# Kernel tuning notes

Measured on AMD Instinct MI355X. Metric: run time of the kernel, lower is better.

Reference implementation:

```python
import jax, jax.numpy as jnp
import numpy as np

NUM_HEADS = 12
LN_EPS = 1e-5


def _layernorm(t, w, b):
    # LayerNorm over last dim (head_dim), biased variance as in torch
    mu = jnp.mean(t, axis=-1, keepdims=True)
    var = jnp.mean(jnp.square(t - mu), axis=-1, keepdims=True)
    return (t - mu) * jax.lax.rsqrt(var + LN_EPS) * w + b


def _apply_rope(t, cos, sin):
    # t: [B, H, S, D]; cos/sin: [S, D//2]; interleaved complex pairs (torch view_as_complex)
    tr = t[..., 0::2]
    ti = t[..., 1::2]
    c = cos[None, None, :, :]
    s = sin[None, None, :, :]
    out_r = tr * c - ti * s
    out_i = tr * s + ti * c
    return jnp.stack([out_r, out_i], axis=-1).reshape(t.shape)


def setup_inputs() -> dict:
    key = jax.random.key(0)
    ks = jax.random.split(key, 6)
    B, N, C = 16, 1024, 768
    H = NUM_HEADS
    D = C // H  # 64
    P, L = 1, 32
    rot_len = N - P - L  # 991
    x = jax.random.normal(ks[0], (B, N, C), dtype=jnp.float32)
    # rotary frequencies (llama-style)
    inv_freq = 1.0 / (10000.0 ** (np.arange(0, D, 2, dtype=np.float32) / D))
    angles = np.arange(rot_len, dtype=np.float32)[:, None] * inv_freq[None, :]
    cos = jnp.asarray(np.cos(angles))
    sin = jnp.asarray(np.sin(angles))
    # parameters (qkv_bias=False, qk_norm=True)
    w_qkv = jax.random.normal(ks[1], (C, 3 * C), dtype=jnp.float32) * (C ** -0.5)
    q_ln_w = jnp.ones((D,), jnp.float32)
    q_ln_b = jnp.zeros((D,), jnp.float32)
    k_ln_w = jnp.ones((D,), jnp.float32)
    k_ln_b = jnp.zeros((D,), jnp.float32)
    w_proj = jax.random.normal(ks[2], (C, C), dtype=jnp.float32) * (C ** -0.5)
    b_proj = jnp.zeros((C,), jnp.float32)
    return {
        "x": x, "cos": cos, "sin": sin,
        "w_qkv": w_qkv,
        "q_ln_w": q_ln_w, "q_ln_b": q_ln_b,
        "k_ln_w": k_ln_w, "k_ln_b": k_ln_b,
        "w_proj": w_proj, "b_proj": b_proj,
        "num_prefix_tokens": 1, "num_latent_tokens": 32,
    }


def reference(x, cos, sin, w_qkv, q_ln_w, q_ln_b, k_ln_w, k_ln_b, w_proj, b_proj,
              num_prefix_tokens, num_latent_tokens):
    B, N, C = x.shape
    H = NUM_HEADS
    D = C // H
    P, L = num_prefix_tokens, num_latent_tokens
    scale = D ** -0.5

    qkv = (x @ w_qkv).reshape(B, N, 3, H, D)
    qkv = jnp.transpose(qkv, (2, 0, 3, 1, 4))  # [3, B, H, N, D]
    q, k, v = qkv[0], qkv[1], qkv[2]

    q = _layernorm(q, q_ln_w, q_ln_b)
    k = _layernorm(k, k_ln_w, k_ln_b)

    # partial RoPE: only the middle [P : N-L] tokens are rotated
    q_rot = _apply_rope(q[:, :, P:N - L], cos, sin)
    k_rot = _apply_rope(k[:, :, P:N - L], cos, sin)
    q = jnp.concatenate([q[:, :, :P], q_rot, q[:, :, N - L:]], axis=2)
    k = jnp.concatenate([k[:, :, :P], k_rot, k[:, :, N - L:]], axis=2)

    attn = jnp.einsum("bhqd,bhkd->bhqk", q * scale, k)
    attn = jax.nn.softmax(attn, axis=-1)
    out = jnp.einsum("bhqk,bhkd->bhqd", attn, v)
    out = jnp.transpose(out, (0, 2, 1, 3)).reshape(B, N, C)
    return out @ w_proj + b_proj
```

## Files before the change

### kernel.cpp

```cpp
#include <hip/hip_runtime.h>
#include <hip/hip_bf16.h>

typedef __attribute__((ext_vector_type(8))) short v8s;
typedef __attribute__((ext_vector_type(4))) short v4s;
typedef __attribute__((ext_vector_type(4))) float f32x4;

__device__ __forceinline__ float bf2f(short s){
  unsigned u = ((unsigned)(unsigned short)s) << 16;
  float f; __builtin_memcpy(&f, &u, 4); return f;
}
__device__ __forceinline__ short f2bf(float f){
  unsigned u; __builtin_memcpy(&u, &f, 4);
  unsigned r = (u + 0x7FFFu + ((u >> 16) & 1u)) >> 16;
  return (short)r;
}
__device__ __forceinline__ unsigned cvtpk(float a, float b){
  unsigned r;
  asm("v_cvt_pk_bf16_f32 %0, %1, %2" : "=v"(r) : "v"(a), "v"(b));
  return r;
}

__device__ __forceinline__ void gload16(const void* g, void* l){
  __builtin_amdgcn_global_load_lds((const __attribute__((address_space(1))) void*)g,
                                   (__attribute__((address_space(3))) void*)l, 16, 0, 0);
}

__global__ __launch_bounds__(256) void k_cast8(const float* __restrict__ in,
                                               short* __restrict__ out, long n){
  long i = ((long)blockIdx.x * 256 + threadIdx.x) * 8;
  long stride = (long)gridDim.x * 256 * 8;
  for (; i < n; i += stride){
    float4 a = *(const float4*)(in + i);
    float4 b = *(const float4*)(in + i + 4);
    v8s v;
    v[0]=f2bf(a.x); v[1]=f2bf(a.y); v[2]=f2bf(a.z); v[3]=f2bf(a.w);
    v[4]=f2bf(b.x); v[5]=f2bf(b.y); v[6]=f2bf(b.z); v[7]=f2bf(b.w);
    *(v8s*)(out + i) = v;
  }
}

__global__ __launch_bounds__(256) void k_tcast(const float* __restrict__ in,
                                               short* __restrict__ out, int R, int Cc){
  __shared__ float T[32][33];
  int tx = threadIdx.x & 31, ty = threadIdx.x >> 5;
  int r0 = blockIdx.x * 32, c0 = blockIdx.y * 32;
  #pragma unroll
  for (int p = 0; p < 4; p++){
    int r = ty + p*8;
    T[r][tx] = in[(long)(r0 + r)*Cc + c0 + tx];
  }
  __syncthreads();
  #pragma unroll
  for (int p = 0; p < 4; p++){
    int r = ty + p*8;
    out[(long)(c0 + r)*R + r0 + tx] = f2bf(T[tx][r]);
  }
}

template<int OUT_MODE>
__global__ __launch_bounds__(256) void k_gemm(const short* __restrict__ A,
                                              const short* __restrict__ Bt,
                                              void* __restrict__ Cout,
                                              const float* __restrict__ bias,
                                              int M, int N, int K){
  __shared__ short As[128*64];
  __shared__ short Bs[128*64];
  int row0 = blockIdx.x * 128, col0 = blockIdx.y * 128;
  int t = threadIdx.x;
  int lane = t & 63, w = t >> 6;
  int g = lane >> 4, r16 = lane & 15;
  int wr = w >> 1, wc = w & 1;
  int rsw = (r16 & 7) << 3;
  int srow = t >> 3;
  int scol = ((t & 7) * 8) ^ ((srow & 7) << 3);
  f32x4 acc[4][4];
  #pragma unroll
  for (int mi = 0; mi < 4; mi++)
    #pragma unroll
    for (int ni = 0; ni < 4; ni++)
      acc[mi][ni] = (f32x4){0.f,0.f,0.f,0.f};

  for (int kt = 0; kt < K; kt += 64){
    #pragma unroll
    for (int p = 0; p < 4; p++){
      int rr = p*32 + srow;
      gload16(&A[(long)(row0 + rr)*K + kt + scol], &As[(p*256 + w*64)*8]);
    }
    #pragma unroll
    for (int p = 0; p < 4; p++){
      int rr = p*32 + srow;
      gload16(&Bt[(long)(col0 + rr)*K + kt + scol], &Bs[(p*256 + w*64)*8]);
    }
    __syncthreads();
    #pragma unroll
    for (int ks = 0; ks < 2; ks++){
      v8s af[4], bfr[4];
      #pragma unroll
      for (int mi = 0; mi < 4; mi++)
        af[mi] = *(const v8s*)&As[(wr*64 + mi*16 + r16)*64 + ((ks*32 + g*8) ^ rsw)];
      #pragma unroll
      for (int ni = 0; ni < 4; ni++)
        bfr[ni] = *(const v8s*)&Bs[(wc*64 + ni*16 + r16)*64 + ((ks*32 + g*8) ^ rsw)];
      __builtin_amdgcn_s_setprio(1);
      #pragma unroll
      for (int mi = 0; mi < 4; mi++)
        #pragma unroll
        for (int ni = 0; ni < 4; ni++)
          acc[mi][ni] = __builtin_amdgcn_mfma_f32_16x16x32_bf16(af[mi], bfr[ni], acc[mi][ni], 0, 0, 0);
      __builtin_amdgcn_s_setprio(0);
    }
    __syncthreads();
  }
  #pragma unroll
  for (int mi = 0; mi < 4; mi++)
    #pragma unroll
    for (int ni = 0; ni < 4; ni++){
      int rbase = row0 + wr*64 + mi*16 + g*4;
      int cc = col0 + wc*64 + ni*16 + r16;
      #pragma unroll
      for (int j = 0; j < 4; j++){
        float v = acc[mi][ni][j];
        if (OUT_MODE == 0)
          ((short*)Cout)[(long)(rbase + j)*N + cc] = f2bf(v);
        else
          ((float*)Cout)[(long)(rbase + j)*N + cc] = v + bias[cc];
      }
    }
}

__global__ __launch_bounds__(256) void k_lnrope(const short* __restrict__ QKV,
     const float* __restrict__ cosT, const float* __restrict__ sinT,
     const float* __restrict__ qw, const float* __restrict__ qb,
     const float* __restrict__ kw, const float* __restrict__ kb,
     short* __restrict__ Qb, short* __restrict__ Kb, short* __restrict__ Vt){
  __shared__ short Vs[64][72];
  int blk = blockIdx.x;
  int ntile = blk & 15, h = (blk >> 4) % 12, b = blk / 192;
  int t = threadIdx.x;
  int tl = t >> 2, ch = t & 3;
  int n = ntile*64 + tl;
  long row = (long)(b*1024 + n) * 2304;
  int d0 = ch * 16;
  long outrow = ((long)(b*12 + h)*1024 + n) * 64;

  #pragma unroll
  for (int sel = 0; sel < 2; sel++){
    const short* src = &QKV[row + sel*768 + h*64 + d0];
    float f[16];
    v8s a0 = *(const v8s*)src;
    v8s a1 = *(const v8s*)(src + 8);
    #pragma unroll
    for (int i = 0; i < 8; i++){ f[i] = bf2f(a0[i]); f[8+i] = bf2f(a1[i]); }
    float s1 = 0.f, s2 = 0.f;
    #pragma unroll
    for (int i = 0; i < 16; i++){ s1 += f[i]; s2 += f[i]*f[i]; }
    s1 += __shfl_xor(s1, 1); s2 += __shfl_xor(s2, 1);
    s1 += __shfl_xor(s1, 2); s2 += __shfl_xor(s2, 2);
    float mu = s1 * (1.0f/64.0f);
    float var = s2 * (1.0f/64.0f) - mu*mu;
    float rs = rsqrtf(var + 1e-5f);
    const float* wp = sel ? kw : qw;
    const float* bp = sel ? kb : qb;
    #pragma unroll
    for (int i = 0; i < 16; i++) f[i] = (f[i] - mu)*rs*wp[d0+i] + bp[d0+i];
    if (n >= 1 && n < 992){
      int pos = n - 1;
      const float* cp = &cosT[pos*32 + ch*8];
      const float* sp = &sinT[pos*32 + ch*8];
      #pragma unroll
      for (int i = 0; i < 8; i++){
        float c = cp[i], s = sp[i];
        float tr = f[2*i], ti = f[2*i+1];
        f[2*i]   = tr*c - ti*s;
        f[2*i+1] = tr*s + ti*c;
      }
    }
    if (sel == 0){
      #pragma unroll
      for (int i = 0; i < 16; i++) f[i] *= 0.18033688011112042f;
    }
    v8s o0, o1;
    #pragma unroll
    for (int i = 0; i < 8; i++){ o0[i] = f2bf(f[i]); o1[i] = f2bf(f[8+i]); }
    short* dst = sel ? &Kb[outrow + d0] : &Qb[outrow + d0];
    *(v8s*)dst = o0;
    *(v8s*)(dst + 8) = o1;
  }
  {
    const short* vsrc = &QKV[row + 1536 + h*64 + d0];
    *(v8s*)&Vs[tl][d0]     = *(const v8s*)vsrc;
    *(v8s*)&Vs[tl][d0 + 8] = *(const v8s*)(vsrc + 8);
  }
  __syncthreads();
  {
    int d = tl, nch = ch;
    v8s o0, o1;
    #pragma unroll
    for (int i = 0; i < 8; i++){ o0[i] = Vs[nch*16 + i][d]; o1[i] = Vs[nch*16 + 8 + i][d]; }
    long vrow = ((long)(b*12 + h)*64 + d)*1024 + ntile*64 + nch*16;
    *(v8s*)&Vt[vrow]     = o0;
    *(v8s*)&Vt[vrow + 8] = o1;
  }
}

__global__ __launch_bounds__(512) void k_attn(const short* __restrict__ Qb,
                                              const short* __restrict__ Kb,
                                              const short* __restrict__ Vt,
                                              short* __restrict__ O){
  __shared__ short Ks[64*64];
  __shared__ short Vts[64*64];
  int blk = blockIdx.x;
  int qt = blk & 7, h = (blk >> 3) % 12, b = blk / 96;
  long bh = b*12 + h;
  int t = threadIdx.x, lane = t & 63, w = t >> 6;
  int g = lane >> 4, r16 = lane & 15;
  int rsw = (r16 & 7) << 3;
  int q0 = qt*128 + w*16;

  int srow = t >> 3;
  int scol = ((t & 7) * 8) ^ ((srow & 7) << 3);
  const short* Ksrc = &Kb[(bh*1024 + srow)*64 + scol];
  const short* Vsrc = &Vt[(bh*64 + srow)*1024 + scol];
  short* KsBase  = &Ks[w*512];
  short* VtsBase = &Vts[w*512];

  v8s bq[2];
  #pragma unroll
  for (int tt = 0; tt < 2; tt++)
    bq[tt] = *(const v8s*)&Qb[(bh*1024 + q0 + r16)*64 + tt*32 + g*8];

  f32x4 oacc[4];
  #pragma unroll
  for (int t2 = 0; t2 < 4; t2++) oacc[t2] = (f32x4){0.f,0.f,0.f,0.f};
  float m_run = -1e30f, l_run = 0.f;

  for (int kt = 0; kt < 1024; kt += 64){
    gload16(Ksrc + kt*64, KsBase);
    gload16(Vsrc + kt,    VtsBase);
    __syncthreads();

    f32x4 sacc[4];
    #pragma unroll
    for (int f = 0; f < 4; f++) sacc[f] = (f32x4){0.f,0.f,0.f,0.f};
    #pragma unroll
    for (int tt = 0; tt < 2; tt++){
      v8s ak[4];
      #pragma unroll
      for (int f = 0; f < 4; f++)
        ak[f] = *(const v8s*)&Ks[(f*16 + r16)*64 + ((tt*32 + g*8) ^ rsw)];
      __builtin_amdgcn_s_setprio(1);
      #pragma unroll
      for (int f = 0; f < 4; f++)
        sacc[f] = __builtin_amdgcn_mfma_f32_16x16x32_bf16(ak[f], bq[tt], sacc[f], 0, 0, 0);
      __builtin_amdgcn_s_setprio(0);
    }
    float mt = -1e30f;
    #pragma unroll
    for (int f = 0; f < 4; f++)
      #pragma unroll
      for (int j = 0; j < 4; j++) mt = fmaxf(mt, sacc[f][j]);
    mt = fmaxf(mt, __shfl_xor(mt, 16));
    mt = fmaxf(mt, __shfl_xor(mt, 32));
    float m_new = fmaxf(m_run, mt);
    float alpha = exp2f(m_run - m_new);
    float p[4][4];
    float lsum = 0.f;
    #pragma unroll
    for (int f = 0; f < 4; f++)
      #pragma unroll
      for (int j = 0; j < 4; j++){
        p[f][j] = exp2f(sacc[f][j] - m_new);
        lsum += p[f][j];
      }
    lsum += __shfl_xor(lsum, 16);
    lsum += __shfl_xor(lsum, 32);
    l_run = l_run*alpha + lsum;
    m_run = m_new;
    float aj4[4];
    #pragma unroll
    for (int j = 0; j < 4; j++) aj4[j] = __shfl(alpha, 4*g + j, 64);
    #pragma unroll
    for (int t2 = 0; t2 < 4; t2++)
      #pragma unroll
      for (int j = 0; j < 4; j++) oacc[t2][j] *= aj4[j];

    unsigned d00 = cvtpk(p[0][0], p[0][1]), d01 = cvtpk(p[0][2], p[0][3]);
    unsigned d10 = cvtpk(p[1][0], p[1][1]), d11 = cvtpk(p[1][2], p[1][3]);
    unsigned d20 = cvtpk(p[2][0], p[2][1]), d21 = cvtpk(p[2][2], p[2][3]);
    unsigned d30 = cvtpk(p[3][0], p[3][1]), d31 = cvtpk(p[3][2], p[3][3]);
    union PU { v8s s; unsigned u[4]; };
    PU pa0, pa1;
    pa0.u[0]=d00; pa0.u[1]=d01; pa0.u[2]=d10; pa0.u[3]=d11;
    pa1.u[0]=d20; pa1.u[1]=d21; pa1.u[2]=d30; pa1.u[3]=d31;

    #pragma unroll
    for (int t2 = 0; t2 < 4; t2++){
      int vrow = (t2*16 + r16)*64;
      #pragma unroll
      for (int kb = 0; kb < 2; kb++){
        union VU { v8s s; v4s h[2]; } vb;
        vb.h[0] = *(const v4s*)&Vts[vrow + ((kb*32 + g*4) ^ rsw)];
        vb.h[1] = *(const v4s*)&Vts[vrow + ((kb*32 + 16 + g*4) ^ rsw)];
        __builtin_amdgcn_s_setprio(1);
        oacc[t2] = __builtin_amdgcn_mfma_f32_16x16x32_bf16(kb ? pa1.s : pa0.s, vb.s, oacc[t2], 0, 0, 0);
        __builtin_amdgcn_s_setprio(0);
      }
    }
    __syncthreads();
  }
  float linv = 1.0f / l_run;
  float lj[4];
  #pragma unroll
  for (int j = 0; j < 4; j++) lj[j] = __shfl(linv, 4*g + j, 64);
  #pragma unroll
  for (int t2 = 0; t2 < 4; t2++)
    #pragma unroll
    for (int j = 0; j < 4; j++){
      float v = oacc[t2][j] * lj[j];
      O[((long)b*1024 + q0 + 4*g + j)*768 + h*64 + t2*16 + r16] = f2bf(v);
    }
}

extern "C" void kernel_launch(void* const* d_in, const int* in_sizes, int n_in,
                              void* d_out, int out_size, void* d_ws, size_t ws_size,
                              hipStream_t stream) {
  const float* x      = (const float*)d_in[0];
  const float* cosT   = (const float*)d_in[1];
  const float* sinT   = (const float*)d_in[2];
  const float* w_qkv  = (const float*)d_in[3];
  const float* q_ln_w = (const float*)d_in[4];
  const float* q_ln_b = (const float*)d_in[5];
  const float* k_ln_w = (const float*)d_in[6];
  const float* k_ln_b = (const float*)d_in[7];
  const float* w_proj = (const float*)d_in[8];
  const float* b_proj = (const float*)d_in[9];

  char* ws = (char*)d_ws;
  short* Xb       = (short*)(ws);
  short* Wqkv_bt  = (short*)(ws + 25165824);
  short* Wproj_bt = (short*)(ws + 28704768);
  short* QKV      = (short*)(ws + 29884416);
  short* Qb       = (short*)(ws + 105381888);
  short* Kb       = (short*)(ws + 130547712);
  short* Vt       = (short*)(ws + 155713536);
  short* O        = (short*)(ws + 180879360);

  k_cast8<<<6144, 256, 0, stream>>>(x, Xb, 12582912L);
  k_tcast<<<dim3(24, 72), 256, 0, stream>>>(w_qkv, Wqkv_bt, 768, 2304);
  k_tcast<<<dim3(24, 24), 256, 0, stream>>>(w_proj, Wproj_bt, 768, 768);
  k_gemm<0><<<dim3(128, 18), 256, 0, stream>>>(Xb, Wqkv_bt, QKV, nullptr, 16384, 2304, 768);
  k_lnrope<<<3072, 256, 0, stream>>>(QKV, cosT, sinT, q_ln_w, q_ln_b, k_ln_w, k_ln_b, Qb, Kb, Vt);
  k_attn<<<1536, 512, 0, stream>>>(Qb, Kb, Vt, O);
  k_gemm<1><<<dim3(128, 6), 256, 0, stream>>>(O, Wproj_bt, d_out, b_proj, 16384, 768, 768);
}
```

Before: 360.0 us.

## Double-buffer K/V tiles in attention and skip rescaling when max grows little

The attention kernel now keeps two LDS buffers for K and V. It prefetches the next tile with async global-to-LDS loads while the current tile is computed, so each iteration needs a single barrier instead of load-then-sync. It also adds a lazy-rescale path: the running max and output rescale are updated only when some lane's tile max exceeds the running max by more than 8 (in exp2 units). The max and sum reductions are rewritten as trees. The cost is double the LDS, and p values up to 2^8 in bf16, which could affect accuracy.

```diff
diff --git a/kernel.cpp b/kernel.cpp
--- a/kernel.cpp
+++ b/kernel.cpp
@@ -207,8 +207,8 @@
                                               const short* __restrict__ Kb,
                                               const short* __restrict__ Vt,
                                               short* __restrict__ O){
-  __shared__ short Ks[64*64];
-  __shared__ short Vts[64*64];
+  __shared__ short Ks[2][64*64];
+  __shared__ short Vts[2][64*64];
   int blk = blockIdx.x;
   int qt = blk & 7, h = (blk >> 3) % 12, b = blk / 96;
   long bh = b*12 + h;
@@ -221,8 +221,10 @@
   int scol = ((t & 7) * 8) ^ ((srow & 7) << 3);
   const short* Ksrc = &Kb[(bh*1024 + srow)*64 + scol];
   const short* Vsrc = &Vt[(bh*64 + srow)*1024 + scol];
-  short* KsBase  = &Ks[w*512];
-  short* VtsBase = &Vts[w*512];
+  int lbase = w*512;
+
+  gload16(Ksrc, &Ks[0][lbase]);
+  gload16(Vsrc, &Vts[0][lbase]);
 
   v8s bq[2];
   #pragma unroll
@@ -234,10 +236,19 @@
   for (int t2 = 0; t2 < 4; t2++) oacc[t2] = (f32x4){0.f,0.f,0.f,0.f};
   float m_run = -1e30f, l_run = 0.f;
 
-  for (int kt = 0; kt < 1024; kt += 64){
-    gload16(Ksrc + kt*64, KsBase);
-    gload16(Vsrc + kt,    VtsBase);
-    __syncthreads();
+  asm volatile("s_waitcnt vmcnt(0)" ::: "memory");
+  __builtin_amdgcn_s_barrier();
+  asm volatile("" ::: "memory");
+
+  for (int it = 0; it < 16; ++it){
+    int cur = it & 1;
+    if (it < 15){
+      int kt = (it + 1) * 64;
+      gload16(Ksrc + (long)kt*64, &Ks[cur^1][lbase]);
+      gload16(Vsrc + kt,          &Vts[cur^1][lbase]);
+    }
+    const short* KsC  = &Ks[cur][0];
+    const short* VtsC = &Vts[cur][0];
 
     f32x4 sacc[4];
     #pragma unroll
@@ -247,42 +258,45 @@
       v8s ak[4];
       #pragma unroll
       for (int f = 0; f < 4; f++)
-        ak[f] = *(const v8s*)&Ks[(f*16 + r16)*64 + ((tt*32 + g*8) ^ rsw)];
+        ak[f] = *(const v8s*)&KsC[(f*16 + r16)*64 + ((tt*32 + g*8) ^ rsw)];
       __builtin_amdgcn_s_setprio(1);
       #pragma unroll
       for (int f = 0; f < 4; f++)
         sacc[f] = __builtin_amdgcn_mfma_f32_16x16x32_bf16(ak[f], bq[tt], sacc[f], 0, 0, 0);
       __builtin_amdgcn_s_setprio(0);
     }
-    float mt = -1e30f;
+    float mf[4];
     #pragma unroll
     for (int f = 0; f < 4; f++)
-      #pragma unroll
-      for (int j = 0; j < 4; j++) mt = fmaxf(mt, sacc[f][j]);
+      mf[f] = fmaxf(fmaxf(sacc[f][0], sacc[f][1]), fmaxf(sacc[f][2], sacc[f][3]));
+    float mt = fmaxf(fmaxf(mf[0], mf[1]), fmaxf(mf[2], mf[3]));
     mt = fmaxf(mt, __shfl_xor(mt, 16));
     mt = fmaxf(mt, __shfl_xor(mt, 32));
-    float m_new = fmaxf(m_run, mt);
-    float alpha = exp2f(m_run - m_new);
+    if (!__all(mt - m_run <= 8.0f)){
+      float m_new = fmaxf(m_run, mt);
+      float alpha = exp2f(m_run - m_new);
+      float aj4[4];
+      #pragma unroll
+      for (int j = 0; j < 4; j++) aj4[j] = __shfl(alpha, 4*g + j, 64);
+      #pragma unroll
+      for (int t2 = 0; t2 < 4; t2++)
+        #pragma unroll
+        for (int j = 0; j < 4; j++) oacc[t2][j] *= aj4[j];
+      l_run *= alpha;
+      m_run = m_new;
+    }
     float p[4][4];
-    float lsum = 0.f;
-    #pragma unroll
-    for (int f = 0; f < 4; f++)
-      #pragma unroll
-      for (int j = 0; j < 4; j++){
-        p[f][j] = exp2f(sacc[f][j] - m_new);
-        lsum += p[f][j];
-      }
+    float ls[4];
+    #pragma unroll
+    for (int f = 0; f < 4; f++){
+      #pragma unroll
+      for (int j = 0; j < 4; j++) p[f][j] = exp2f(sacc[f][j] - m_run);
+      ls[f] = (p[f][0] + p[f][1]) + (p[f][2] + p[f][3]);
+    }
+    float lsum = (ls[0] + ls[1]) + (ls[2] + ls[3]);
     lsum += __shfl_xor(lsum, 16);
     lsum += __shfl_xor(lsum, 32);
-    l_run = l_run*alpha + lsum;
-    m_run = m_new;
-    float aj4[4];
-    #pragma unroll
-    for (int j = 0; j < 4; j++) aj4[j] = __shfl(alpha, 4*g + j, 64);
-    #pragma unroll
-    for (int t2 = 0; t2 < 4; t2++)
-      #pragma unroll
-      for (int j = 0; j < 4; j++) oacc[t2][j] *= aj4[j];
+    l_run += lsum;
 
     unsigned d00 = cvtpk(p[0][0], p[0][1]), d01 = cvtpk(p[0][2], p[0][3]);
     unsigned d10 = cvtpk(p[1][0], p[1][1]), d11 = cvtpk(p[1][2], p[1][3]);
@@ -299,14 +313,16 @@
       #pragma unroll
       for (int kb = 0; kb < 2; kb++){
         union VU { v8s s; v4s h[2]; } vb;
-        vb.h[0] = *(const v4s*)&Vts[vrow + ((kb*32 + g*4) ^ rsw)];
-        vb.h[1] = *(const v4s*)&Vts[vrow + ((kb*32 + 16 + g*4) ^ rsw)];
+        vb.h[0] = *(const v4s*)&VtsC[vrow + ((kb*32 + g*4) ^ rsw)];
+        vb.h[1] = *(const v4s*)&VtsC[vrow + ((kb*32 + 16 + g*4) ^ rsw)];
         __builtin_amdgcn_s_setprio(1);
         oacc[t2] = __builtin_amdgcn_mfma_f32_16x16x32_bf16(kb ? pa1.s : pa0.s, vb.s, oacc[t2], 0, 0, 0);
         __builtin_amdgcn_s_setprio(0);
       }
     }
-    __syncthreads();
+    asm volatile("s_waitcnt vmcnt(0)" ::: "memory");
+    __builtin_amdgcn_s_barrier();
+    asm volatile("" ::: "memory");
   }
   float linv = 1.0f / l_run;
   float lj[4];
```

Result: no change. 363.9 us (+1.1%).
